# Kernel tuning notes

Hardware: AMD Instinct MI355X
Metric: run time of the kernel (lower is better)

## Reference

```python
import jax, jax.numpy as jnp
import numpy as np

N_NODES = 50000
N_EDGES = 800000
N_FEAT = 128
N_HID = 128
N_LAYER = 4
N_CLASS = 40


def setup_inputs() -> dict:
    key = jax.random.key(0)
    ks = jax.random.split(key, 8)
    x = jax.random.normal(ks[0], (N_NODES, N_FEAT), jnp.float32)
    edge_index = jax.random.randint(ks[1], (2, N_EDGES), 0, N_NODES, dtype=jnp.int64)
    s = 1.0 / np.float32(np.sqrt(N_HID))
    # n_feat == n_hid so all L conv weights stack into one [L, C, C] tensor
    convW = jax.random.normal(ks[2], (N_LAYER, N_HID, N_HID), jnp.float32) * s
    convb = jnp.zeros((N_LAYER, N_HID), jnp.float32)
    W_att = jax.random.normal(ks[3], (N_HID, N_HID), jnp.float32) * s
    a_att = jax.random.normal(ks[4], (N_HID,), jnp.float32) * s
    W_out = jax.random.normal(ks[5], (N_HID, N_CLASS), jnp.float32) * s
    b_out = jnp.zeros((N_CLASS,), jnp.float32)
    return dict(x=x, edge_index=edge_index, convW=convW, convb=convb,
                W_att=W_att, a_att=a_att, W_out=W_out, b_out=b_out)


def reference(x, edge_index, convW, convb, W_att, a_att, W_out, b_out):
    src, dst = edge_index[0], edge_index[1]
    N = x.shape[0]
    # GCN symmetric normalization with self-loops: deg = 1 + in-degree
    deg = jax.ops.segment_sum(jnp.ones_like(dst, dtype=jnp.float32), dst,
                              num_segments=N) + 1.0
    dinv = jax.lax.rsqrt(deg)
    enorm = (dinv[src] * dinv[dst])[:, None]   # per-edge norm
    snorm = (dinv * dinv)[:, None]             # self-loop norm

    hs = []
    h = x
    for l in range(N_LAYER):
        hW = h @ convW[l]                                          # [N, C]
        agg = jax.ops.segment_sum(hW[src] * enorm, dst, num_segments=N)
        agg = agg + hW * snorm                                     # self-loop
        h = jax.nn.relu(agg + convb[l])
        # dropout is identity at inference (training=False)
        hs.append(h)

    H = jnp.stack(hs, axis=1)                                      # [N, L, C]
    # additive attention over layers: alpha_l = softmax_l(a . tanh(W h_l))
    scores = jnp.tanh(H @ W_att) @ a_att                           # [N, L]
    alpha = jax.nn.softmax(scores, axis=1)
    fused = jnp.einsum('nl,nlc->nc', alpha, H)                     # [N, C]
    return fused @ W_out + b_out                                   # [N, n_class]
```

## Files before the change

kernel.cpp:

```cpp
#include <hip/hip_runtime.h>

#define NNODES 50000
#define NEDGES 800000
#define NCLASS 40
#define GEMMB 782
#define XBLK  3125
#define WELL  64

#define EBLK  782
#define PREPB 80
#define WOUTB 6
#define BSHIFT 10
#define NB    49
#define BUCKCAP 20480

typedef _Float16 half8  __attribute__((ext_vector_type(8)));
typedef float    floatx4 __attribute__((ext_vector_type(4)));

#define CSTR 136
#define SMEM_BYTES (64 * CSTR * 2 + 256)

__device__ __forceinline__ float fast_tanh(float x) {
    return 1.0f - 2.0f / (__expf(2.0f * x) + 1.0f);
}

__global__ __launch_bounds__(1024) void k_part(const int* __restrict__ src, const int* __restrict__ dst,
                                               int* __restrict__ gbase, unsigned int* __restrict__ ebuf,
                                               const float* __restrict__ convW, const float* __restrict__ W_att,
                                               _Float16* __restrict__ WT,
                                               const float* __restrict__ Wout, _Float16* __restrict__ WoutT) {
    int bid = blockIdx.x, tid = threadIdx.x;
    if (bid < EBLK) {
        __shared__ int hist[NB];
        __shared__ int base[NB];
        if (tid < NB) hist[tid] = 0;
        __syncthreads();
        int e = bid * 1024 + tid;
        bool ok = e < NEDGES;
        int s = 0, d = 0, b = 0, slot = 0;
        if (ok) {
            d = dst[e];
            s = src[e];
            b = d >> BSHIFT;
            slot = atomicAdd(&hist[b], 1);
        }
        __syncthreads();
        if (tid < NB) base[tid] = atomicAdd(&gbase[tid * 32], hist[tid]);
        __syncthreads();
        if (ok) {
            int pos = base[b] + slot;
            unsigned int packed = ((unsigned int)(d & ((1 << BSHIFT) - 1)) << 16) | (unsigned int)s;
            if (pos < BUCKCAP) ebuf[(size_t)b * BUCKCAP + pos] = packed;
        }
    } else if (bid < EBLK + PREPB) {
        int idx = (bid - EBLK) * 1024 + tid;
        int mat = idx >> 14, rem = idx & 16383;
        int j = rem & 7, lane = (rem >> 3) & 63, tile = rem >> 9;
        int l15 = lane & 15, quad = lane >> 4;
        int ct = tile & 7, kk = tile >> 3;
        int n = ct * 16 + l15, k = kk * 32 + quad * 8 + j;
        const float* s = (mat < 4) ? (convW + mat * 16384) : W_att;
        WT[idx] = (_Float16)s[k * 128 + n];
    } else {
        int idx = (bid - EBLK - PREPB) * 1024 + tid;
        int j = idx & 7, lane = (idx >> 3) & 63, tile = idx >> 9;
        int l15 = lane & 15, quad = lane >> 4;
        int ct = tile % 3, kk = tile / 3;
        int n = ct * 16 + l15, k = kk * 32 + quad * 8 + j;
        WoutT[idx] = (n < NCLASS) ? (_Float16)Wout[k * NCLASS + n] : (_Float16)0.f;
    }
}

__global__ __launch_bounds__(1024) void k_build(const int* __restrict__ gbase,
                                                const unsigned int* __restrict__ ebuf,
                                                int* __restrict__ esrc, int* __restrict__ cnt) {
    __shared__ int lcnt[1024];
    int b = blockIdx.x, t = threadIdx.x;
    lcnt[t] = 0;
    __syncthreads();
    int n0 = b << BSHIFT;
    int total = gbase[b * 32];
    if (total > BUCKCAP) total = BUCKCAP;
    const unsigned int* ep = ebuf + (size_t)b * BUCKCAP;
    for (int i = t; i < total; i += 1024) {
        unsigned int p = ep[i];
        int doff = (int)(p >> 16);
        int s = (int)(p & 0xFFFFu);
        int slot = atomicAdd(&lcnt[doff], 1);
        if (slot < WELL) esrc[(n0 + doff) * WELL + slot] = s;
    }
    __syncthreads();
    int n = n0 + t;
    if (n < NNODES) cnt[n] = (lcnt[t] < WELL) ? lcnt[t] : WELL;
}

__global__ __launch_bounds__(256) void k_gemm0(const float* __restrict__ Av, const _Float16* __restrict__ WTf,
                                               const int* __restrict__ cnt, _Float16* __restrict__ C) {
    __shared__ __align__(16) char smem[SMEM_BYTES];
    _Float16 (*Csh)[CSTR] = (_Float16 (*)[CSTR])smem;
    float* sdinv = (float*)(smem + 64 * CSTR * 2);
    int m0 = blockIdx.x * 64;
    int tid = threadIdx.x;
    int wave = tid >> 6, lane = tid & 63;
    int quad = lane >> 4, l15 = lane & 15;
    int ko = quad * 8;

    if (tid < 64) {
        int r = m0 + tid; if (r > NNODES - 1) r = NNODES - 1;
        sdinv[tid] = rsqrtf((float)cnt[r] + 1.0f);
    }

    floatx4 acc[4][2];
#pragma unroll
    for (int rt = 0; rt < 4; ++rt)
#pragma unroll
        for (int ct = 0; ct < 2; ++ct) acc[rt][ct] = (floatx4){0.f, 0.f, 0.f, 0.f};

#pragma unroll
    for (int kk = 0; kk < 4; ++kk) {
        half8 a[4], b[2];
#pragma unroll
        for (int rt = 0; rt < 4; ++rt) {
            int row = m0 + rt * 16 + l15;
            if (row > NNODES - 1) row = NNODES - 1;
            const float* Ap = Av + (size_t)row * 128 + kk * 32 + ko;
            float4 f0 = *(const float4*)Ap;
            float4 f1 = *(const float4*)(Ap + 4);
            a[rt] = (half8){(_Float16)f0.x, (_Float16)f0.y, (_Float16)f0.z, (_Float16)f0.w,
                            (_Float16)f1.x, (_Float16)f1.y, (_Float16)f1.z, (_Float16)f1.w};
        }
#pragma unroll
        for (int ct = 0; ct < 2; ++ct)
            b[ct] = *(const half8*)&WTf[((kk * 8 + (wave * 2 + ct)) * 64 + lane) * 8];
#pragma unroll
        for (int rt = 0; rt < 4; ++rt)
#pragma unroll
            for (int ct = 0; ct < 2; ++ct)
                acc[rt][ct] = __builtin_amdgcn_mfma_f32_16x16x32_f16(a[rt], b[ct], acc[rt][ct], 0, 0, 0);
    }
    __syncthreads();

#pragma unroll
    for (int rt = 0; rt < 4; ++rt)
#pragma unroll
        for (int r = 0; r < 4; ++r) {
            float d = sdinv[rt * 16 + quad * 4 + r];
#pragma unroll
            for (int ct = 0; ct < 2; ++ct)
                Csh[rt * 16 + quad * 4 + r][wave * 32 + ct * 16 + l15] = (_Float16)(acc[rt][ct][r] * d);
        }
    __syncthreads();

    int row = tid >> 2, seg = tid & 3;
    int gm = m0 + row;
    if (gm < NNODES) {
#pragma unroll
        for (int j = 0; j < 4; ++j)
            *(half8*)(C + (size_t)gm * 128 + seg * 32 + j * 8) = *(const half8*)&Csh[row][seg * 32 + j * 8];
    }
}

__global__ __launch_bounds__(128) void k_layer(const _Float16* __restrict__ hin,
                                               const int* __restrict__ cnt, const int* __restrict__ esrc,
                                               const float* __restrict__ bias,
                                               _Float16* __restrict__ hh,
                                               const _Float16* __restrict__ WTatt, const float* __restrict__ a_att,
                                               float* __restrict__ scores, int layer,
                                               const _Float16* __restrict__ WTnext, _Float16* __restrict__ hout) {
    __shared__ __align__(16) _Float16 h[16][CSTR];
    __shared__ float bsh[128];
    __shared__ float sdv[16];
    __shared__ float pp[2][16];
    int tid = threadIdx.x;
    bsh[tid] = bias[tid];
    int wave = tid >> 6, lane = tid & 63;
    int n0 = blockIdx.x * 16;

    {
        int nl = tid >> 3;
        int cl = tid & 7;
        int c16 = cl * 16;
        int n = n0 + nl;
        int cv = cnt[n];
        int beg = n * WELL, end = beg + cv;
        float dn = rsqrtf((float)cv + 1.0f);
        const _Float16* sp = hin + (size_t)n * 128 + c16;
        half8 sv0 = *(const half8*)sp;
        half8 sv1 = *(const half8*)(sp + 8);

        float a[16];
#pragma unroll
        for (int u = 0; u < 16; ++u) a[u] = 0.f;

        int idxA[4]; float mskA[4];
#pragma unroll
        for (int i = 0; i < 4; ++i) {
            int ei = beg + i;
            int t = esrc[ei];
            bool ok = ei < end;
            idxA[i] = ok ? t : n;
            mskA[i] = ok ? 1.f : 0.f;
        }
        for (int e = beg; e < end; e += 4) {
            half8 v0[4], v1[4];
#pragma unroll
            for (int i = 0; i < 4; ++i) {
                const _Float16* p = hin + (size_t)idxA[i] * 128 + c16;
                v0[i] = *(const half8*)p;
                v1[i] = *(const half8*)(p + 8);
            }
            int idxB[4]; float mskB[4];
#pragma unroll
            for (int i = 0; i < 4; ++i) {
                int ei = e + 4 + i;
                int t = esrc[ei];
                bool ok = ei < end;
                idxB[i] = ok ? t : n;
                mskB[i] = ok ? 1.f : 0.f;
            }
#pragma unroll
            for (int i = 0; i < 4; ++i) {
                float m = mskA[i];
#pragma unroll
                for (int u = 0; u < 8; ++u) {
                    a[u]     += m * (float)v0[i][u];
                    a[8 + u] += m * (float)v1[i][u];
                }
            }
#pragma unroll
            for (int i = 0; i < 4; ++i) { idxA[i] = idxB[i]; mskA[i] = mskB[i]; }
        }
        __syncthreads();
        half8 o0, o1;
#pragma unroll
        for (int u = 0; u < 8; ++u) {
            float r0 = (a[u]     + (float)sv0[u]) * dn + bsh[c16 + u];
            float r1 = (a[8 + u] + (float)sv1[u]) * dn + bsh[c16 + 8 + u];
            o0[u] = (_Float16)fmaxf(r0, 0.f);
            o1[u] = (_Float16)fmaxf(r1, 0.f);
        }
        *(half8*)(hh + (size_t)n * 128 + c16)     = o0;
        *(half8*)(hh + (size_t)n * 128 + c16 + 8) = o1;
        *(half8*)&h[nl][c16]     = o0;
        *(half8*)&h[nl][c16 + 8] = o1;
        if (cl == 0) sdv[nl] = dn;
    }
    __syncthreads();

    int quad = lane >> 4, l15 = lane & 15;
    int ko = quad * 8;
    half8 af[4];
#pragma unroll
    for (int kk = 0; kk < 4; ++kk) af[kk] = *(const half8*)&h[l15][kk * 32 + ko];

    {
        float p[4] = {0.f, 0.f, 0.f, 0.f};
#pragma unroll
        for (int c2 = 0; c2 < 4; ++c2) {
            int ct = wave * 4 + c2;
            half8 b[4];
#pragma unroll
            for (int kk = 0; kk < 4; ++kk)
                b[kk] = *(const half8*)&WTatt[((kk * 8 + ct) * 64 + lane) * 8];
            floatx4 acc = (floatx4){0.f, 0.f, 0.f, 0.f};
#pragma unroll
            for (int kk = 0; kk < 4; ++kk)
                acc = __builtin_amdgcn_mfma_f32_16x16x32_f16(af[kk], b[kk], acc, 0, 0, 0);
            float av = a_att[ct * 16 + l15];
#pragma unroll
            for (int r = 0; r < 4; ++r) p[r] += av * fast_tanh(acc[r]);
        }
#pragma unroll
        for (int r = 0; r < 4; ++r) {
            float v = p[r];
            v += __shfl_xor(v, 1); v += __shfl_xor(v, 2);
            v += __shfl_xor(v, 4); v += __shfl_xor(v, 8);
            if (l15 == 0) pp[wave][quad * 4 + r] = v;
        }
    }
    __syncthreads();
    if (tid < 16) scores[(size_t)(n0 + tid) * 4 + layer] = pp[0][tid] + pp[1][tid];

    {
        floatx4 acc[4];
#pragma unroll
        for (int c2 = 0; c2 < 4; ++c2) acc[c2] = (floatx4){0.f, 0.f, 0.f, 0.f};
#pragma unroll
        for (int c2 = 0; c2 < 4; ++c2) {
            int ct = wave * 4 + c2;
#pragma unroll
            for (int kk = 0; kk < 4; ++kk) {
                half8 b = *(const half8*)&WTnext[((kk * 8 + ct) * 64 + lane) * 8];
                acc[c2] = __builtin_amdgcn_mfma_f32_16x16x32_f16(af[kk], b, acc[c2], 0, 0, 0);
            }
        }
        __syncthreads();
#pragma unroll
        for (int c2 = 0; c2 < 4; ++c2) {
            int col = wave * 64 + c2 * 16 + l15;
#pragma unroll
            for (int r = 0; r < 4; ++r) {
                int row = quad * 4 + r;
                h[row][col] = (_Float16)(acc[c2][r] * sdv[row]);
            }
        }
        __syncthreads();
        int row = tid >> 3, seg = tid & 7;
        int gm = n0 + row;
        *(half8*)(hout + (size_t)gm * 128 + seg * 16)     = *(const half8*)&h[row][seg * 16];
        *(half8*)(hout + (size_t)gm * 128 + seg * 16 + 8) = *(const half8*)&h[row][seg * 16 + 8];
    }
}

__global__ __launch_bounds__(128) void k_layer_last(const _Float16* __restrict__ hin,
                                                    const int* __restrict__ cnt, const int* __restrict__ esrc,
                                                    const float* __restrict__ bias,
                                                    const _Float16* __restrict__ WTatt,
                                                    const float* __restrict__ a_att,
                                                    const float* __restrict__ scores,
                                                    const _Float16* __restrict__ h0g,
                                                    const _Float16* __restrict__ h1g,
                                                    const _Float16* __restrict__ h2g,
                                                    const _Float16* __restrict__ WoutT,
                                                    const float* __restrict__ bout,
                                                    float* __restrict__ out) {
    __shared__ __align__(16) _Float16 h[16][CSTR];
    __shared__ float bsh[128];
    __shared__ float pp[2][16];
    int tid = threadIdx.x;
    bsh[tid] = bias[tid];
    int wave = tid >> 6, lane = tid & 63;
    int n0 = blockIdx.x * 16;
    int nl = tid >> 3, cl = tid & 7, c16 = cl * 16;
    int n = n0 + nl;

    {
        int cv = cnt[n];
        int beg = n * WELL, end = beg + cv;
        float dn = rsqrtf((float)cv + 1.0f);
        const _Float16* sp = hin + (size_t)n * 128 + c16;
        half8 sv0 = *(const half8*)sp;
        half8 sv1 = *(const half8*)(sp + 8);

        float a[16];
#pragma unroll
        for (int u = 0; u < 16; ++u) a[u] = 0.f;

        int idxA[4]; float mskA[4];
#pragma unroll
        for (int i = 0; i < 4; ++i) {
            int ei = beg + i;
            int t = esrc[ei];
            bool ok = ei < end;
            idxA[i] = ok ? t : n;
            mskA[i] = ok ? 1.f : 0.f;
        }
        for (int e = beg; e < end; e += 4) {
            half8 v0[4], v1[4];
#pragma unroll
            for (int i = 0; i < 4; ++i) {
                const _Float16* p = hin + (size_t)idxA[i] * 128 + c16;
                v0[i] = *(const half8*)p;
                v1[i] = *(const half8*)(p + 8);
            }
            int idxB[4]; float mskB[4];
#pragma unroll
            for (int i = 0; i < 4; ++i) {
                int ei = e + 4 + i;
                int t = esrc[ei];
                bool ok = ei < end;
                idxB[i] = ok ? t : n;
                mskB[i] = ok ? 1.f : 0.f;
            }
#pragma unroll
            for (int i = 0; i < 4; ++i) {
                float m = mskA[i];
#pragma unroll
                for (int u = 0; u < 8; ++u) {
                    a[u]     += m * (float)v0[i][u];
                    a[8 + u] += m * (float)v1[i][u];
                }
            }
#pragma unroll
            for (int i = 0; i < 4; ++i) { idxA[i] = idxB[i]; mskA[i] = mskB[i]; }
        }
        __syncthreads();
        half8 o0, o1;
#pragma unroll
        for (int u = 0; u < 8; ++u) {
            float r0 = (a[u]     + (float)sv0[u]) * dn + bsh[c16 + u];
            float r1 = (a[8 + u] + (float)sv1[u]) * dn + bsh[c16 + 8 + u];
            o0[u] = (_Float16)fmaxf(r0, 0.f);
            o1[u] = (_Float16)fmaxf(r1, 0.f);
        }
        *(half8*)&h[nl][c16]     = o0;
        *(half8*)&h[nl][c16 + 8] = o1;
    }
    __syncthreads();

    int quad = lane >> 4, l15 = lane & 15;
    int ko = quad * 8;

    {
        half8 af[4];
#pragma unroll
        for (int kk = 0; kk < 4; ++kk) af[kk] = *(const half8*)&h[l15][kk * 32 + ko];
        float p[4] = {0.f, 0.f, 0.f, 0.f};
#pragma unroll
        for (int c2 = 0; c2 < 4; ++c2) {
            int ct = wave * 4 + c2;
            half8 b[4];
#pragma unroll
            for (int kk = 0; kk < 4; ++kk)
                b[kk] = *(const half8*)&WTatt[((kk * 8 + ct) * 64 + lane) * 8];
            floatx4 acc = (floatx4){0.f, 0.f, 0.f, 0.f};
#pragma unroll
            for (int kk = 0; kk < 4; ++kk)
                acc = __builtin_amdgcn_mfma_f32_16x16x32_f16(af[kk], b[kk], acc, 0, 0, 0);
            float av = a_att[ct * 16 + l15];
#pragma unroll
            for (int r = 0; r < 4; ++r) p[r] += av * fast_tanh(acc[r]);
        }
#pragma unroll
        for (int r = 0; r < 4; ++r) {
            float v = p[r];
            v += __shfl_xor(v, 1); v += __shfl_xor(v, 2);
            v += __shfl_xor(v, 4); v += __shfl_xor(v, 8);
            if (l15 == 0) pp[wave][quad * 4 + r] = v;
        }
    }
    __syncthreads();

    {
        float s0 = scores[(size_t)n * 4 + 0];
        float s1 = scores[(size_t)n * 4 + 1];
        float s2 = scores[(size_t)n * 4 + 2];
        float s3 = pp[0][nl] + pp[1][nl];
        float mx = fmaxf(fmaxf(s0, s1), fmaxf(s2, s3));
        float e0 = __expf(s0 - mx), e1 = __expf(s1 - mx), e2 = __expf(s2 - mx), e3 = __expf(s3 - mx);
        float inv = 1.0f / (e0 + e1 + e2 + e3);
        float al0 = e0 * inv, al1 = e1 * inv, al2 = e2 * inv, al3 = e3 * inv;

        const _Float16* p0 = h0g + (size_t)n * 128 + c16;
        const _Float16* p1 = h1g + (size_t)n * 128 + c16;
        const _Float16* p2 = h2g + (size_t)n * 128 + c16;
        half8 a0 = *(const half8*)p0, b0 = *(const half8*)(p0 + 8);
        half8 a1 = *(const half8*)p1, b1 = *(const half8*)(p1 + 8);
        half8 a2 = *(const half8*)p2, b2 = *(const half8*)(p2 + 8);
        half8 a3 = *(const half8*)&h[nl][c16], b3 = *(const half8*)&h[nl][c16 + 8];
        half8 f0, f1;
#pragma unroll
        for (int u = 0; u < 8; ++u) {
            f0[u] = (_Float16)(al0 * (float)a0[u] + al1 * (float)a1[u] +
                               al2 * (float)a2[u] + al3 * (float)a3[u]);
            f1[u] = (_Float16)(al0 * (float)b0[u] + al1 * (float)b1[u] +
                               al2 * (float)b2[u] + al3 * (float)b3[u]);
        }
        __syncthreads();
        *(half8*)&h[nl][c16]     = f0;
        *(half8*)&h[nl][c16 + 8] = f1;
    }
    __syncthreads();

    {
        half8 ff[4];
#pragma unroll
        for (int kk = 0; kk < 4; ++kk) ff[kk] = *(const half8*)&h[l15][kk * 32 + ko];
        int nct = (wave == 0) ? 2 : 1;
#pragma unroll
        for (int c2 = 0; c2 < 2; ++c2) {
            if (c2 >= nct) break;
            int ct = (wave == 0) ? c2 : 2;
            half8 bw[4];
#pragma unroll
            for (int kk = 0; kk < 4; ++kk)
                bw[kk] = *(const half8*)(WoutT + ((kk * 3 + ct) * 64 + lane) * 8);
            floatx4 acc = (floatx4){0.f, 0.f, 0.f, 0.f};
#pragma unroll
            for (int kk = 0; kk < 4; ++kk)
                acc = __builtin_amdgcn_mfma_f32_16x16x32_f16(ff[kk], bw[kk], acc, 0, 0, 0);
            int col = ct * 16 + l15;
            if (col < NCLASS) {
                float bv = bout[col];
#pragma unroll
                for (int r = 0; r < 4; ++r) {
                    int node = n0 + quad * 4 + r;
                    out[(size_t)node * NCLASS + col] = acc[r] + bv;
                }
            }
        }
    }
}

extern "C" void kernel_launch(void* const* d_in, const int* in_sizes, int n_in,
                              void* d_out, int out_size, void* d_ws, size_t ws_size,
                              hipStream_t stream) {
    const float* x     = (const float*)d_in[0];
    const int*   ei    = (const int*)d_in[1];
    const float* convW = (const float*)d_in[2];
    const float* convb = (const float*)d_in[3];
    const float* W_att = (const float*)d_in[4];
    const float* a_att = (const float*)d_in[5];
    const float* W_out = (const float*)d_in[6];
    const float* b_out = (const float*)d_in[7];
    float* out = (float*)d_out;

    char* ws = (char*)d_ws;
    size_t off = 0;
    auto take = [&](size_t nbytes) { char* p = ws + off; off += (nbytes + 255) & ~(size_t)255; return p; };
    int*          cnt     = (int*)take(NNODES * 4);
    int*          gbase   = (int*)take((size_t)NB * 32 * 4);
    unsigned int* ebuf    = (unsigned int*)take((size_t)NB * BUCKCAP * 4);
    int*          esrc    = (int*)take((size_t)NNODES * WELL * 4 + 1024);
    _Float16*     WoutT   = (_Float16*)take((size_t)48 * 128 * 2);
    float*        scores  = (float*)take(NNODES * 4 * 4);
    _Float16*     WT      = (_Float16*)take((size_t)5 * 128 * 128 * 2);
    _Float16*     hWsA    = (_Float16*)take((size_t)NNODES * 128 * 2);
    _Float16*     hh[3];
    for (int l = 0; l < 3; ++l) hh[l] = (_Float16*)take((size_t)NNODES * 128 * 2);
    _Float16*     hWsB    = (_Float16*)take((size_t)NNODES * 128 * 2);

    const int* src = ei;
    const int* dst = ei + NEDGES;

    hipMemsetAsync(gbase, 0, (size_t)NB * 32 * 4, stream);
    k_part<<<EBLK + PREPB + WOUTB, 1024, 0, stream>>>(src, dst, gbase, ebuf, convW, W_att, WT, W_out, WoutT);
    k_build<<<NB, 1024, 0, stream>>>(gbase, ebuf, esrc, cnt);
    k_gemm0<<<GEMMB, 256, 0, stream>>>(x, WT, cnt, hWsA);

    k_layer<<<XBLK, 128, 0, stream>>>(hWsA, cnt, esrc, convb + 0 * 128, hh[0],
                                      WT + 4 * 16384, a_att, scores, 0, WT + 1 * 16384, hWsB);
    k_layer<<<XBLK, 128, 0, stream>>>(hWsB, cnt, esrc, convb + 1 * 128, hh[1],
                                      WT + 4 * 16384, a_att, scores, 1, WT + 2 * 16384, hWsA);
    k_layer<<<XBLK, 128, 0, stream>>>(hWsA, cnt, esrc, convb + 2 * 128, hh[2],
                                      WT + 4 * 16384, a_att, scores, 2, WT + 3 * 16384, hWsB);
    k_layer_last<<<XBLK, 128, 0, stream>>>(hWsB, cnt, esrc, convb + 3 * 128,
                                           WT + 4 * 16384, a_att, scores,
                                           hh[0], hh[1], hh[2], WoutT, b_out, out);
}
```

Measured before the change: 286.4 us.

## Coalesce bucket scatter via LDS staging and split CSR build across quarter-buckets

```diff
diff --git a/kernel.cpp b/kernel.cpp
--- a/kernel.cpp
+++ b/kernel.cpp
@@ -32,25 +32,44 @@
     int bid = blockIdx.x, tid = threadIdx.x;
     if (bid < EBLK) {
         __shared__ int hist[NB];
+        __shared__ int lofs[NB + 1];
         __shared__ int base[NB];
+        __shared__ unsigned int stage[1024];
         if (tid < NB) hist[tid] = 0;
         __syncthreads();
         int e = bid * 1024 + tid;
         bool ok = e < NEDGES;
-        int s = 0, d = 0, b = 0, slot = 0;
+        int b = 0, slot = 0;
+        unsigned int packed = 0;
         if (ok) {
-            d = dst[e];
-            s = src[e];
+            int d = dst[e];
+            int s = src[e];
             b = d >> BSHIFT;
             slot = atomicAdd(&hist[b], 1);
-        }
-        __syncthreads();
+            packed = ((unsigned int)(d & ((1 << BSHIFT) - 1)) << 16) | (unsigned int)s;
+        }
+        __syncthreads();
+        if (tid < 64) {
+            int v = (tid < NB) ? hist[tid] : 0;
+            int inc = v;
+#pragma unroll
+            for (int d2 = 1; d2 < 64; d2 <<= 1) {
+                int o = __shfl_up(inc, d2);
+                if (tid >= d2) inc += o;
+            }
+            if (tid < NB) lofs[tid] = inc - v;
+            if (tid == NB - 1) lofs[NB] = inc;
+        }
         if (tid < NB) base[tid] = atomicAdd(&gbase[tid * 32], hist[tid]);
         __syncthreads();
-        if (ok) {
-            int pos = base[b] + slot;
-            unsigned int packed = ((unsigned int)(d & ((1 << BSHIFT) - 1)) << 16) | (unsigned int)s;
-            if (pos < BUCKCAP) ebuf[(size_t)b * BUCKCAP + pos] = packed;
+        if (ok) stage[lofs[b] + slot] = packed;
+        __syncthreads();
+        int total = lofs[NB];
+        if (tid < total) {
+            int lo = 0, hi = NB;
+            while (hi - lo > 1) { int mid = (lo + hi) >> 1; if (lofs[mid] <= tid) lo = mid; else hi = mid; }
+            int pos = base[lo] + (tid - lofs[lo]);
+            if (pos < BUCKCAP) ebuf[(size_t)lo * BUCKCAP + pos] = stage[tid];
         }
     } else if (bid < EBLK + PREPB) {
         int idx = (bid - EBLK) * 1024 + tid;
@@ -74,9 +93,10 @@
 __global__ __launch_bounds__(1024) void k_build(const int* __restrict__ gbase,
                                                 const unsigned int* __restrict__ ebuf,
                                                 int* __restrict__ esrc, int* __restrict__ cnt) {
-    __shared__ int lcnt[1024];
-    int b = blockIdx.x, t = threadIdx.x;
-    lcnt[t] = 0;
+    __shared__ int lcnt[256];
+    int b = blockIdx.x >> 2, q = blockIdx.x & 3;
+    int t = threadIdx.x;
+    if (t < 256) lcnt[t] = 0;
     __syncthreads();
     int n0 = b << BSHIFT;
     int total = gbase[b * 32];
@@ -85,13 +105,16 @@
     for (int i = t; i < total; i += 1024) {
         unsigned int p = ep[i];
         int doff = (int)(p >> 16);
-        int s = (int)(p & 0xFFFFu);
-        int slot = atomicAdd(&lcnt[doff], 1);
-        if (slot < WELL) esrc[(n0 + doff) * WELL + slot] = s;
-    }
-    __syncthreads();
-    int n = n0 + t;
-    if (n < NNODES) cnt[n] = (lcnt[t] < WELL) ? lcnt[t] : WELL;
+        if ((doff >> 8) == q) {
+            int slot = atomicAdd(&lcnt[doff & 255], 1);
+            if (slot < WELL) esrc[(n0 + doff) * WELL + slot] = (int)(p & 0xFFFFu);
+        }
+    }
+    __syncthreads();
+    if (t < 256) {
+        int n = n0 + (q << 8) + t;
+        if (n < NNODES) cnt[n] = (lcnt[t] < WELL) ? lcnt[t] : WELL;
+    }
 }
 
 __global__ __launch_bounds__(256) void k_gemm0(const float* __restrict__ Av, const _Float16* __restrict__ WTf,
@@ -331,7 +354,7 @@
     bsh[tid] = bias[tid];
     int wave = tid >> 6, lane = tid & 63;
     int n0 = blockIdx.x * 16;
-    int nl = tid >> 3, cl = tid & 7, c16 = cl * 16;
+    int nl = tid >> 3, cl = tid & 7, c16 = cl * 8 * 2;
     int n = n0 + nl;
 
     {
@@ -525,7 +548,7 @@
 
     hipMemsetAsync(gbase, 0, (size_t)NB * 32 * 4, stream);
     k_part<<<EBLK + PREPB + WOUTB, 1024, 0, stream>>>(src, dst, gbase, ebuf, convW, W_att, WT, W_out, WoutT);
-    k_build<<<NB, 1024, 0, stream>>>(gbase, ebuf, esrc, cnt);
+    k_build<<<NB * 4, 1024, 0, stream>>>(gbase, ebuf, esrc, cnt);
     k_gemm0<<<GEMMB, 256, 0, stream>>>(x, WT, cnt, hWsA);
 
     k_layer<<<XBLK, 128, 0, stream>>>(hWsA, cnt, esrc, convb + 0 * 128, hh[0],
```

Measured after the change: 281.3 us. About the same (-1.8%).
